# Kernel tuning notes

Measured on AMD Instinct MI355X. Metric: run time of the kernel, lower is better.

## Reference

```python
import jax, jax.numpy as jnp
import numpy as np

N, E = 50000, 800000
IN, HID, L, HEADS, OUT = 128, 256, 8, 8, 40
DH = HID // HEADS


def setup_inputs() -> dict:
    key = jax.random.key(0)
    ks = jax.random.split(key, 12)
    s = 0.05
    d = {}
    d["X"] = jax.random.normal(ks[0], (N, IN), jnp.float32)
    d["src"] = jax.random.randint(ks[1], (E,), 0, N, dtype=jnp.int32)
    d["dst"] = jax.random.randint(ks[2], (E,), 0, N, dtype=jnp.int32)
    d["Win"] = jax.random.normal(ks[3], (IN, HID), jnp.float32) * s
    d["bin_"] = jnp.zeros((HID,), jnp.float32)
    d["Wq"] = jax.random.normal(ks[4], (L, HID, HID), jnp.float32) * s
    d["Wk"] = jax.random.normal(ks[5], (L, HID, HID), jnp.float32) * s
    d["Wv"] = jax.random.normal(ks[6], (L, HID, HID), jnp.float32) * s
    d["bq"] = jnp.zeros((L, HID), jnp.float32)
    d["bk"] = jnp.zeros((L, HID), jnp.float32)
    d["bv"] = jnp.zeros((L, HID), jnp.float32)
    d["Wout"] = jax.random.normal(ks[7], (HID, OUT), jnp.float32) * s
    d["bout"] = jnp.zeros((OUT,), jnp.float32)
    return d


def _segment_softmax(e, seg, n):
    # e: [E, H] edge scores, seg: [E] destination node ids
    m = jax.ops.segment_max(e, seg, num_segments=n)
    ex = jnp.exp(e - m[seg])
    s = jax.ops.segment_sum(ex, seg, num_segments=n)
    return ex / s[seg]


def reference(X, src, dst, Win, bin_, Wq, Wk, Wv, bq, bk, bv, Wout, bout):
    n = X.shape[0]
    scaling = DH ** -0.5
    h = X @ Win + bin_  # in_proj: [N, HID]
    for l in range(L):  # fixed small layer stack
        q = (h @ Wq[l] + bq[l]).reshape(n, HEADS, DH) * scaling
        k = (h @ Wk[l] + bk[l]).reshape(n, HEADS, DH)
        v = (h @ Wv[l] + bv[l]).reshape(n, HEADS, DH)
        # SDDMM: per-edge, per-head dot product q[dst] . k[src]
        e = jnp.einsum('ehd,ehd->eh', q[dst], k[src])  # [E, HEADS]
        a = _segment_softmax(e, dst, n)                # softmax over in-edges of each dst
        # SpMM: weighted aggregation of source values into destinations
        h = jax.ops.segment_sum(a[..., None] * v[src], dst, num_segments=n).reshape(n, HID)
    return h @ Wout + bout  # predictor: [N, OUT]
```

## Files before the change

### kernel.cpp

```cpp
#include <hip/hip_runtime.h>
#include <hip/hip_bf16.h>
#include <hip/hip_fp16.h>

#define N_NODES 50000
#define MPAD    50048
#define N_EDGES 800000
#define IN_DIM  128
#define HID     256
#define QKVW    768
#define N_LAYERS 8
#define OUT_DIM 40
#define SCALING 0.17677669529663687f

typedef __attribute__((ext_vector_type(8))) _Float16 f16x8;
typedef __attribute__((ext_vector_type(4))) float f32x4;

__device__ __forceinline__ void gload_lds16(const void* g, void* l) {
    __builtin_amdgcn_global_load_lds(
        (__attribute__((address_space(1))) const unsigned int*)g,
        (__attribute__((address_space(3))) unsigned int*)l, 16, 0, 0);
}

__global__ void hist_kernel(const int* __restrict__ dst, int* __restrict__ cnt, int E) {
    int e = blockIdx.x * blockDim.x + threadIdx.x;
    if (e < E) atomicAdd(&cnt[dst[e]], 1);
}

__global__ __launch_bounds__(1024) void scan_kernel(const int* __restrict__ cnt,
                                                    int* __restrict__ row_off, int n) {
    __shared__ int wsum[16];
    __shared__ int carry_s;
    int tid = threadIdx.x;
    int lane = tid & 63, wid = tid >> 6;
    if (tid == 0) carry_s = 0;
    __syncthreads();
    for (int base = 0; base < n; base += 1024) {
        int i = base + tid;
        int x = (i < n) ? cnt[i] : 0;
        int v = x;
#pragma unroll
        for (int off = 1; off < 64; off <<= 1) {
            int y = __shfl_up(v, off);
            if (lane >= off) v += y;
        }
        if (lane == 63) wsum[wid] = v;
        __syncthreads();
        if (wid == 0) {
            int w = (lane < 16) ? wsum[lane] : 0;
#pragma unroll
            for (int off = 1; off < 16; off <<= 1) {
                int y = __shfl_up(w, off);
                if (lane >= off) w += y;
            }
            if (lane < 16) wsum[lane] = w;
        }
        __syncthreads();
        int wbase = (wid > 0) ? wsum[wid - 1] : 0;
        int carry = carry_s;
        if (i < n) row_off[i] = carry + wbase + v - x;
        int total = wsum[15];
        __syncthreads();
        if (tid == 0) carry_s = carry + total;
        __syncthreads();
    }
    if (tid == 0) row_off[n] = carry_s;
}

__global__ void scatter_kernel(const int* __restrict__ src, const int* __restrict__ dst,
                               const int* __restrict__ row_off, int* __restrict__ cur,
                               int* __restrict__ csr_src, int E) {
    int e = blockIdx.x * blockDim.x + threadIdx.x;
    if (e < E) {
        int d = dst[e];
        int pos = row_off[d] + atomicAdd(&cur[d], 1);
        csr_src[pos] = src[e];
    }
}

__global__ void wqkv_cvt_kernel(const float* __restrict__ Wq, const float* __restrict__ Wk,
                                const float* __restrict__ Wv, _Float16* __restrict__ outw) {
    int i = blockIdx.x * blockDim.x + threadIdx.x;
    if (i >= N_LAYERS * QKVW * HID) return;
    int k = i & 255;
    int n = (i >> 8) % QKVW;
    int l = i / (QKVW * HID);
    int seg = n >> 8, nn = n & 255;
    const float* W = (seg == 0) ? Wq : (seg == 1) ? Wk : Wv;
    outw[i] = (_Float16)W[((size_t)l * HID + k) * HID + nn];
}

__global__ void win_cvt_kernel(const float* __restrict__ Win, _Float16* __restrict__ outw) {
    int i = blockIdx.x * blockDim.x + threadIdx.x;
    if (i >= HID * IN_DIM) return;
    int k = i & 127;
    int n = i >> 7;
    outw[i] = (_Float16)Win[(size_t)k * HID + n];
}

__global__ void wout_cvt_kernel(const float* __restrict__ Wout, _Float16* __restrict__ hi,
                                _Float16* __restrict__ lo) {
    int i = blockIdx.x * blockDim.x + threadIdx.x;
    if (i >= 128 * HID) return;
    int k = i & 255;
    int n = i >> 8;
    float v = (n < OUT_DIM) ? Wout[(size_t)k * OUT_DIM + n] : 0.f;
    _Float16 h = (_Float16)v;
    hi[i] = h;
    lo[i] = (_Float16)(v - (float)h);
}

__global__ void x_cvt_kernel(const float* __restrict__ X, _Float16* __restrict__ outx) {
    int i = blockIdx.x * blockDim.x + threadIdx.x;
    if (i >= MPAD * IN_DIM) return;
    int r = i >> 7;
    outx[i] = (_Float16)((r < N_NODES) ? X[i] : 0.f);
}

template<int NT>
__global__ __launch_bounds__(256) void gemm16(
        const _Float16* __restrict__ A, const _Float16* __restrict__ B,
        const float* __restrict__ bias0, const float* __restrict__ bias1,
        const float* __restrict__ bias2, float scale0,
        _Float16* __restrict__ C, int ldC) {
    __shared__ __align__(16) _Float16 lds[2][2 * 4096];
    const int K = NT * 32;

    const int tid  = threadIdx.x;
    const int lane = tid & 63;
    const int wave = tid >> 6;
    const int row0 = blockIdx.x * 128;
    const int n0   = blockIdx.y * 128;

    const int p0 = wave * 64 + lane;
    const int p1 = p0 + 256;
    auto srcoff = [&](int p, int grow0) -> size_t {
        int row = p >> 2, cir = p & 3;
        int sw  = (row & 3) ^ ((row >> 2) & 3);
        int sc  = cir ^ sw;
        return (size_t)(grow0 + row) * K + sc * 8;
    };
    const size_t offA0 = srcoff(p0, row0), offA1 = srcoff(p1, row0);
    const size_t offB0 = srcoff(p0, n0),   offB1 = srcoff(p1, n0);
    const int d0 = wave * 512;
    const int d1 = 2048 + wave * 512;

    const int mh = (wave >> 1) * 64;
    const int nh = (wave & 1) * 64;
    int aoff[4], boff[4];
#pragma unroll
    for (int f = 0; f < 4; ++f) {
        int ra = mh + f * 16 + (lane & 15);
        int ca = (lane >> 4) ^ ((ra & 3) ^ ((ra >> 2) & 3));
        aoff[f] = ra * 64 + ca * 16;
        int rb = nh + f * 16 + (lane & 15);
        int cb = (lane >> 4) ^ ((rb & 3) ^ ((rb >> 2) & 3));
        boff[f] = rb * 64 + cb * 16;
    }

    f32x4 acc[4][4];
#pragma unroll
    for (int i = 0; i < 4; ++i)
#pragma unroll
        for (int j = 0; j < 4; ++j) acc[i][j] = {0.f, 0.f, 0.f, 0.f};

    auto STAGE = [&](int b, int t) {
        _Float16* LA = &lds[b][0];
        _Float16* LB = &lds[b][4096];
        const size_t k0 = (size_t)t * 32;
        gload_lds16(A + offA0 + k0, LA + d0);
        gload_lds16(A + offA1 + k0, LA + d1);
        gload_lds16(B + offB0 + k0, LB + d0);
        gload_lds16(B + offB1 + k0, LB + d1);
    };

    STAGE(0, 0);
#pragma unroll
    for (int t = 0; t < NT; ++t) {
        const int cur = t & 1;
        if (t + 1 < NT) {
            STAGE(cur ^ 1, t + 1);
            asm volatile("s_waitcnt vmcnt(4)" ::: "memory");
        } else {
            asm volatile("s_waitcnt vmcnt(0)" ::: "memory");
        }
        __builtin_amdgcn_s_barrier();
        const char* baseA = (const char*)&lds[cur][0];
        const char* baseB = (const char*)&lds[cur][4096];
        f16x8 af[4];
#pragma unroll
        for (int i = 0; i < 4; ++i)
            af[i] = *reinterpret_cast<const f16x8*>(baseA + aoff[i]);
#pragma unroll
        for (int j = 0; j < 4; ++j) {
            f16x8 bf = *reinterpret_cast<const f16x8*>(baseB + boff[j]);
#pragma unroll
            for (int i = 0; i < 4; ++i)
                acc[i][j] = __builtin_amdgcn_mfma_f32_16x16x32_f16(af[i], bf, acc[i][j], 0, 0, 0);
        }
        __builtin_amdgcn_s_barrier();
    }

    const int seg = n0 >> 8;
    const float* bias = (seg == 0) ? bias0 : (seg == 1) ? bias1 : bias2;
    const float scale = (seg == 0) ? scale0 : 1.f;
    const int fq = lane >> 4;
    const int fr = lane & 15;
#pragma unroll
    for (int i = 0; i < 4; ++i) {
#pragma unroll
        for (int j = 0; j < 4; ++j) {
#pragma unroll
            for (int r = 0; r < 4; ++r) {
                int m = row0 + mh + i * 16 + fq * 4 + r;
                int n = n0 + nh + j * 16 + fr;
                float o = (acc[i][j][r] + bias[n & 255]) * scale;
                C[(size_t)m * ldC + n] = (_Float16)o;
            }
        }
    }
}

__global__ __launch_bounds__(256) void gemm_out(
        const _Float16* __restrict__ A, const _Float16* __restrict__ Bh,
        const _Float16* __restrict__ Bl, const float* __restrict__ bias,
        float* __restrict__ C, int K) {
    __shared__ __align__(16) _Float16 lds[2][3 * 4096];

    const int tid  = threadIdx.x;
    const int lane = tid & 63;
    const int wave = tid >> 6;
    const int row0 = blockIdx.x * 128;

    const int p0 = wave * 64 + lane;
    const int p1 = p0 + 256;
    auto srcoff = [&](int p, int grow0) -> size_t {
        int row = p >> 2, cir = p & 3;
        int sw  = (row & 3) ^ ((row >> 2) & 3);
        int sc  = cir ^ sw;
        return (size_t)(grow0 + row) * K + sc * 8;
    };
    const size_t offA0 = srcoff(p0, row0), offA1 = srcoff(p1, row0);
    const size_t offB0 = srcoff(p0, 0),    offB1 = srcoff(p1, 0);
    const int d0 = wave * 512;
    const int d1 = 2048 + wave * 512;

    const int mh = (wave >> 1) * 64;
    const int nh = (wave & 1) * 64;
    int aoff[4], boff[4];
#pragma unroll
    for (int f = 0; f < 4; ++f) {
        int ra = mh + f * 16 + (lane & 15);
        int ca = (lane >> 4) ^ ((ra & 3) ^ ((ra >> 2) & 3));
        aoff[f] = ra * 64 + ca * 16;
        int rb = nh + f * 16 + (lane & 15);
        int cb = (lane >> 4) ^ ((rb & 3) ^ ((rb >> 2) & 3));
        boff[f] = rb * 64 + cb * 16;
    }

    f32x4 acc[4][4];
#pragma unroll
    for (int i = 0; i < 4; ++i)
#pragma unroll
        for (int j = 0; j < 4; ++j) acc[i][j] = {0.f, 0.f, 0.f, 0.f};

    auto STAGE = [&](int b, int t) {
        _Float16* LA  = &lds[b][0];
        _Float16* LBh = &lds[b][4096];
        _Float16* LBl = &lds[b][8192];
        const size_t k0 = (size_t)t * 32;
        gload_lds16(A  + offA0 + k0, LA  + d0);
        gload_lds16(A  + offA1 + k0, LA  + d1);
        gload_lds16(Bh + offB0 + k0, LBh + d0);
        gload_lds16(Bh + offB1 + k0, LBh + d1);
        gload_lds16(Bl + offB0 + k0, LBl + d0);
        gload_lds16(Bl + offB1 + k0, LBl + d1);
    };

    STAGE(0, 0);
#pragma unroll
    for (int t = 0; t < 8; ++t) {
        const int cur = t & 1;
        if (t + 1 < 8) {
            STAGE(cur ^ 1, t + 1);
            asm volatile("s_waitcnt vmcnt(6)" ::: "memory");
        } else {
            asm volatile("s_waitcnt vmcnt(0)" ::: "memory");
        }
        __builtin_amdgcn_s_barrier();
        const char* baseA  = (const char*)&lds[cur][0];
        const char* baseBh = (const char*)&lds[cur][4096];
        const char* baseBl = (const char*)&lds[cur][8192];
        f16x8 af[4];
#pragma unroll
        for (int i = 0; i < 4; ++i)
            af[i] = *reinterpret_cast<const f16x8*>(baseA + aoff[i]);
#pragma unroll
        for (int j = 0; j < 4; ++j) {
            f16x8 bh = *reinterpret_cast<const f16x8*>(baseBh + boff[j]);
            f16x8 bl = *reinterpret_cast<const f16x8*>(baseBl + boff[j]);
#pragma unroll
            for (int i = 0; i < 4; ++i) {
                acc[i][j] = __builtin_amdgcn_mfma_f32_16x16x32_f16(af[i], bh, acc[i][j], 0, 0, 0);
                acc[i][j] = __builtin_amdgcn_mfma_f32_16x16x32_f16(af[i], bl, acc[i][j], 0, 0, 0);
            }
        }
        __builtin_amdgcn_s_barrier();
    }

    const int fq = lane >> 4;
    const int fr = lane & 15;
#pragma unroll
    for (int i = 0; i < 4; ++i) {
#pragma unroll
        for (int j = 0; j < 4; ++j) {
#pragma unroll
            for (int r = 0; r < 4; ++r) {
                int m = row0 + mh + i * 16 + fq * 4 + r;
                int n = nh + j * 16 + fr;
                if (m < N_NODES && n < OUT_DIM)
                    C[(size_t)m * OUT_DIM + n] = acc[i][j][r] + bias[n];
            }
        }
    }
}

__global__ __launch_bounds__(256) void attn_kernel(
        const _Float16* __restrict__ qkv, const int* __restrict__ row_off,
        const int* __restrict__ csr_src, _Float16* __restrict__ h_out, int n) {
    int wave = threadIdx.x >> 6;
    int lane = threadIdx.x & 63;
    int node = blockIdx.x * 4 + wave;
    if (node >= n) return;
    const int loff = lane * 4;
    float4 qv;
    {
        float2 raw = *reinterpret_cast<const float2*>(&qkv[(size_t)node * QKVW + loff]);
        const __half2* h2 = reinterpret_cast<const __half2*>(&raw);
        float2 a = __half22float2(h2[0]), b = __half22float2(h2[1]);
        qv = make_float4(a.x, a.y, b.x, b.y);
    }
    float4 acc = make_float4(0.f, 0.f, 0.f, 0.f);
    float m = -INFINITY, s = 0.f;
    int beg = row_off[node], end = row_off[node + 1];
    int idx = beg;

#define LOAD_KV(slot, sn)                                                                 \
    float2 kr##slot, vr##slot;                                                            \
    {                                                                                     \
        const _Float16* base = qkv + (size_t)(sn) * QKVW;                                 \
        kr##slot = *reinterpret_cast<const float2*>(base + HID + loff);                   \
        vr##slot = *reinterpret_cast<const float2*>(base + 2 * HID + loff);               \
    }

#define DOT(slot, dvar)                                                                   \
    float dvar;                                                                           \
    {                                                                                     \
        const __half2* kh = reinterpret_cast<const __half2*>(&kr##slot);                  \
        float2 k01 = __half22float2(kh[0]), k23 = __half22float2(kh[1]);                  \
        dvar = qv.x * k01.x + qv.y * k01.y + qv.z * k23.x + qv.w * k23.y;                 \
        dvar += __shfl_xor(dvar, 1);                                                      \
        dvar += __shfl_xor(dvar, 2);                                                      \
        dvar += __shfl_xor(dvar, 4);                                                      \
    }

#define VADD(slot, p)                                                                     \
    {                                                                                     \
        const __half2* vh = reinterpret_cast<const __half2*>(&vr##slot);                  \
        float2 v01 = __half22float2(vh[0]), v23 = __half22float2(vh[1]);                  \
        acc.x = fmaf(p, v01.x, acc.x);                                                    \
        acc.y = fmaf(p, v01.y, acc.y);                                                    \
        acc.z = fmaf(p, v23.x, acc.z);                                                    \
        acc.w = fmaf(p, v23.y, acc.w);                                                    \
    }

    for (; idx + 3 < end; idx += 4) {
        int s0 = csr_src[idx], s1 = csr_src[idx + 1];
        int s2 = csr_src[idx + 2], s3 = csr_src[idx + 3];
        LOAD_KV(0, s0) LOAD_KV(1, s1) LOAD_KV(2, s2) LOAD_KV(3, s3)
        DOT(0, e0) DOT(1, e1) DOT(2, e2) DOT(3, e3)
        float mn = fmaxf(fmaxf(fmaxf(m, e0), fmaxf(e1, e2)), e3);
        float c  = __expf(m - mn);
        float p0 = __expf(e0 - mn), p1 = __expf(e1 - mn);
        float p2 = __expf(e2 - mn), p3 = __expf(e3 - mn);
        s = fmaf(s, c, (p0 + p1) + (p2 + p3));
        acc.x *= c; acc.y *= c; acc.z *= c; acc.w *= c;
        VADD(0, p0) VADD(1, p1) VADD(2, p2) VADD(3, p3)
        m = mn;
    }
    for (; idx < end; ++idx) {
        int s0 = csr_src[idx];
        LOAD_KV(0, s0)
        DOT(0, e0)
        float mn = fmaxf(m, e0);
        float c = __expf(m - mn);
        float p0 = __expf(e0 - mn);
        s = fmaf(s, c, p0);
        acc.x *= c; acc.y *= c; acc.z *= c; acc.w *= c;
        VADD(0, p0)
        m = mn;
    }
#undef LOAD_KV
#undef DOT
#undef VADD

    float inv = (s > 0.f) ? 1.f / s : 0.f;
    __half2 o01 = __floats2half2_rn(acc.x * inv, acc.y * inv);
    __half2 o23 = __floats2half2_rn(acc.z * inv, acc.w * inv);
    union { __half2 h2[2]; float2 f2; } u;
    u.h2[0] = o01; u.h2[1] = o23;
    *reinterpret_cast<float2*>(&h_out[(size_t)node * HID + loff]) = u.f2;
}

extern "C" void kernel_launch(void* const* d_in, const int* in_sizes, int n_in,
                              void* d_out, int out_size, void* d_ws, size_t ws_size,
                              hipStream_t stream) {
    const float* X    = (const float*)d_in[0];
    const int*   src  = (const int*)d_in[1];
    const int*   dst  = (const int*)d_in[2];
    const float* Win  = (const float*)d_in[3];
    const float* bin_ = (const float*)d_in[4];
    const float* Wq   = (const float*)d_in[5];
    const float* Wk   = (const float*)d_in[6];
    const float* Wv   = (const float*)d_in[7];
    const float* bq   = (const float*)d_in[8];
    const float* bk   = (const float*)d_in[9];
    const float* bv   = (const float*)d_in[10];
    const float* Wout = (const float*)d_in[11];
    const float* bout = (const float*)d_in[12];
    float* out = (float*)d_out;

    char* ws = (char*)d_ws;
    size_t off = 0;
    auto alloc = [&](size_t bytes) -> void* {
        void* p = ws + off;
        off = (off + bytes + 255) & ~(size_t)255;
        return p;
    };
    _Float16* qkv   = (_Float16*)alloc((size_t)MPAD * QKVW * 2);
    _Float16* h     = (_Float16*)alloc((size_t)MPAD * HID * 2);
    _Float16* Xf    = (_Float16*)alloc((size_t)MPAD * IN_DIM * 2);
    _Float16* Wqkvt = (_Float16*)alloc((size_t)N_LAYERS * QKVW * HID * 2);
    _Float16* Wint  = (_Float16*)alloc((size_t)HID * IN_DIM * 2);
    _Float16* Wot_h = (_Float16*)alloc((size_t)128 * HID * 2);
    _Float16* Wot_l = (_Float16*)alloc((size_t)128 * HID * 2);
    int* cnt     = (int*)alloc(sizeof(int) * N_NODES);
    int* row_off = (int*)alloc(sizeof(int) * (N_NODES + 1));
    int* csr_src = (int*)alloc(sizeof(int) * N_EDGES);

    hipMemsetAsync(cnt, 0, sizeof(int) * N_NODES, stream);
    hist_kernel<<<(N_EDGES + 255) / 256, 256, 0, stream>>>(dst, cnt, N_EDGES);
    scan_kernel<<<1, 1024, 0, stream>>>(cnt, row_off, N_NODES);
    hipMemsetAsync(cnt, 0, sizeof(int) * N_NODES, stream);
    scatter_kernel<<<(N_EDGES + 255) / 256, 256, 0, stream>>>(src, dst, row_off, cnt, csr_src, N_EDGES);

    {
        int t1 = N_LAYERS * QKVW * HID;
        wqkv_cvt_kernel<<<(t1 + 255) / 256, 256, 0, stream>>>(Wq, Wk, Wv, Wqkvt);
        int t2 = HID * IN_DIM;
        win_cvt_kernel<<<(t2 + 255) / 256, 256, 0, stream>>>(Win, Wint);
        int t3 = 128 * HID;
        wout_cvt_kernel<<<(t3 + 255) / 256, 256, 0, stream>>>(Wout, Wot_h, Wot_l);
        int t4 = MPAD * IN_DIM;
        x_cvt_kernel<<<(t4 + 255) / 256, 256, 0, stream>>>(X, Xf);
    }

    dim3 blk(256);
    gemm16<4><<<dim3(MPAD / 128, 2), blk, 0, stream>>>(
        Xf, Wint, bin_, bin_, bin_, 1.f, h, HID);

    for (int l = 0; l < N_LAYERS; ++l) {
        const _Float16* Bl = Wqkvt + (size_t)l * QKVW * HID;
        gemm16<8><<<dim3(MPAD / 128, 6), blk, 0, stream>>>(
            h, Bl, bq + l * HID, bk + l * HID, bv + l * HID, SCALING, qkv, QKVW);
        attn_kernel<<<(N_NODES + 3) / 4, blk, 0, stream>>>(
            qkv, row_off, csr_src, h, N_NODES);
    }
    gemm_out<<<dim3(MPAD / 128, 1), blk, 0, stream>>>(
        h, Wot_h, Wot_l, bout, out, HID);
}
```

Measured before the change: 1.518 ms.

## Interleave K/V columns, sort CSR neighbours by source, remap GEMM block order

The QKV GEMM now writes K and V interleaved per column, so the attention kernel fetches both for a neighbour with one 16-byte load instead of two 8-byte loads. A new resort kernel buckets each node's neighbour list by source-id range (warp ballot) for better gather locality. The GEMM grid is flattened with a swizzle that groups 8 row blocks per column tile, aiming for L2 reuse of B, and padded blocks are skipped. Together these add a preprocessing pass, extra workspace and more complex index math.

Result: no change. 1.526 ms (+0.5%).

```diff
diff --git a/kernel.cpp b/kernel.cpp
--- a/kernel.cpp
+++ b/kernel.cpp
@@ -4,6 +4,7 @@
 
 #define N_NODES 50000
 #define MPAD    50048
+#define NRB     391
 #define N_EDGES 800000
 #define IN_DIM  128
 #define HID     256
@@ -77,6 +78,31 @@
     }
 }
 
+__global__ __launch_bounds__(256) void resort_kernel(
+        const int* __restrict__ row_off, const int* __restrict__ csr_in,
+        int* __restrict__ csr_out, int n) {
+    int wave = threadIdx.x >> 6, lane = threadIdx.x & 63;
+    int node = blockIdx.x * 4 + wave;
+    if (node >= n) return;
+    int beg = row_off[node], end = row_off[node + 1];
+    int deg = end - beg;
+    if (deg <= 64) {
+        int sv = (lane < deg) ? csr_in[beg + lane] : 0;
+        int b  = (lane < deg) ? (sv >> 10) : 63;
+        int base = 0;
+        for (int t = 0; t < 49; ++t) {
+            unsigned long long mask = __ballot(b == t);
+            if (b == t) {
+                int pre = __popcll(mask & ((1ull << lane) - 1ull));
+                csr_out[beg + base + pre] = sv;
+            }
+            base += __popcll(mask);
+        }
+    } else {
+        for (int i = beg + lane; i < end; i += 64) csr_out[i] = csr_in[i];
+    }
+}
+
 __global__ void wqkv_cvt_kernel(const float* __restrict__ Wq, const float* __restrict__ Wk,
                                 const float* __restrict__ Wv, _Float16* __restrict__ outw) {
     int i = blockIdx.x * blockDim.x + threadIdx.x;
@@ -116,7 +142,7 @@
     outx[i] = (_Float16)((r < N_NODES) ? X[i] : 0.f);
 }
 
-template<int NT>
+template<int NT, int NCOLT, bool KVILV>
 __global__ __launch_bounds__(256) void gemm16(
         const _Float16* __restrict__ A, const _Float16* __restrict__ B,
         const float* __restrict__ bias0, const float* __restrict__ bias1,
@@ -125,11 +151,17 @@
     __shared__ __align__(16) _Float16 lds[2][2 * 4096];
     const int K = NT * 32;
 
+    const int bb = blockIdx.x;
+    const int xx = bb & 7, tt = bb >> 3;
+    const int qq = tt / NCOLT, jj = tt - qq * NCOLT;
+    const int rowblk = qq * 8 + xx;
+    if (rowblk >= NRB) return;
+    const int row0 = rowblk * 128;
+    const int n0   = jj * 128;
+
     const int tid  = threadIdx.x;
     const int lane = tid & 63;
     const int wave = tid >> 6;
-    const int row0 = blockIdx.x * 128;
-    const int n0   = blockIdx.y * 128;
 
     const int p0 = wave * 64 + lane;
     const int p1 = p0 + 256;
@@ -214,7 +246,9 @@
                 int m = row0 + mh + i * 16 + fq * 4 + r;
                 int n = n0 + nh + j * 16 + fr;
                 float o = (acc[i][j][r] + bias[n & 255]) * scale;
-                C[(size_t)m * ldC + n] = (_Float16)o;
+                int col = n;
+                if (KVILV && n >= 256) col = 256 + 2 * (n & 255) + (n >= 512 ? 1 : 0);
+                C[(size_t)m * ldC + col] = (_Float16)o;
             }
         }
     }
@@ -322,6 +356,28 @@
             }
         }
     }
+}
+
+struct KVf { float2 p0, p1, p2, p3; };
+__device__ __forceinline__ KVf unpack_kv(const float4& r) {
+    const __half2* h = reinterpret_cast<const __half2*>(&r);
+    KVf o;
+    o.p0 = __half22float2(h[0]); o.p1 = __half22float2(h[1]);
+    o.p2 = __half22float2(h[2]); o.p3 = __half22float2(h[3]);
+    return o;
+}
+__device__ __forceinline__ float dot_kv(const float4& q, const KVf& kv) {
+    float d = q.x * kv.p0.x + q.y * kv.p1.x + q.z * kv.p2.x + q.w * kv.p3.x;
+    d += __shfl_xor(d, 1);
+    d += __shfl_xor(d, 2);
+    d += __shfl_xor(d, 4);
+    return d;
+}
+__device__ __forceinline__ void vadd_kv(float4& acc, float p, const KVf& kv) {
+    acc.x = fmaf(p, kv.p0.y, acc.x);
+    acc.y = fmaf(p, kv.p1.y, acc.y);
+    acc.z = fmaf(p, kv.p2.y, acc.z);
+    acc.w = fmaf(p, kv.p3.y, acc.w);
 }
 
 __global__ __launch_bounds__(256) void attn_kernel(
@@ -343,65 +399,42 @@
     float m = -INFINITY, s = 0.f;
     int beg = row_off[node], end = row_off[node + 1];
     int idx = beg;
-
-#define LOAD_KV(slot, sn)                                                                 \
-    float2 kr##slot, vr##slot;                                                            \
-    {                                                                                     \
-        const _Float16* base = qkv + (size_t)(sn) * QKVW;                                 \
-        kr##slot = *reinterpret_cast<const float2*>(base + HID + loff);                   \
-        vr##slot = *reinterpret_cast<const float2*>(base + 2 * HID + loff);               \
-    }
-
-#define DOT(slot, dvar)                                                                   \
-    float dvar;                                                                           \
-    {                                                                                     \
-        const __half2* kh = reinterpret_cast<const __half2*>(&kr##slot);                  \
-        float2 k01 = __half22float2(kh[0]), k23 = __half22float2(kh[1]);                  \
-        dvar = qv.x * k01.x + qv.y * k01.y + qv.z * k23.x + qv.w * k23.y;                 \
-        dvar += __shfl_xor(dvar, 1);                                                      \
-        dvar += __shfl_xor(dvar, 2);                                                      \
-        dvar += __shfl_xor(dvar, 4);                                                      \
-    }
-
-#define VADD(slot, p)                                                                     \
-    {                                                                                     \
-        const __half2* vh = reinterpret_cast<const __half2*>(&vr##slot);                  \
-        float2 v01 = __half22float2(vh[0]), v23 = __half22float2(vh[1]);                  \
-        acc.x = fmaf(p, v01.x, acc.x);                                                    \
-        acc.y = fmaf(p, v01.y, acc.y);                                                    \
-        acc.z = fmaf(p, v23.x, acc.z);                                                    \
-        acc.w = fmaf(p, v23.y, acc.w);                                                    \
-    }
+    const int koff = HID + 2 * loff;
 
     for (; idx + 3 < end; idx += 4) {
         int s0 = csr_src[idx], s1 = csr_src[idx + 1];
         int s2 = csr_src[idx + 2], s3 = csr_src[idx + 3];
-        LOAD_KV(0, s0) LOAD_KV(1, s1) LOAD_KV(2, s2) LOAD_KV(3, s3)
-        DOT(0, e0) DOT(1, e1) DOT(2, e2) DOT(3, e3)
+        float4 r0 = *(const float4*)(qkv + (size_t)s0 * QKVW + koff);
+        float4 r1 = *(const float4*)(qkv + (size_t)s1 * QKVW + koff);
+        float4 r2 = *(const float4*)(qkv + (size_t)s2 * QKVW + koff);
+        float4 r3 = *(const float4*)(qkv + (size_t)s3 * QKVW + koff);
+        KVf kv0 = unpack_kv(r0), kv1 = unpack_kv(r1);
+        KVf kv2 = unpack_kv(r2), kv3 = unpack_kv(r3);
+        float e0 = dot_kv(qv, kv0), e1 = dot_kv(qv, kv1);
+        float e2 = dot_kv(qv, kv2), e3 = dot_kv(qv, kv3);
         float mn = fmaxf(fmaxf(fmaxf(m, e0), fmaxf(e1, e2)), e3);
         float c  = __expf(m - mn);
         float p0 = __expf(e0 - mn), p1 = __expf(e1 - mn);
         float p2 = __expf(e2 - mn), p3 = __expf(e3 - mn);
         s = fmaf(s, c, (p0 + p1) + (p2 + p3));
         acc.x *= c; acc.y *= c; acc.z *= c; acc.w *= c;
-        VADD(0, p0) VADD(1, p1) VADD(2, p2) VADD(3, p3)
+        vadd_kv(acc, p0, kv0); vadd_kv(acc, p1, kv1);
+        vadd_kv(acc, p2, kv2); vadd_kv(acc, p3, kv3);
         m = mn;
     }
     for (; idx < end; ++idx) {
         int s0 = csr_src[idx];
-        LOAD_KV(0, s0)
-        DOT(0, e0)
+        float4 r0 = *(const float4*)(qkv + (size_t)s0 * QKVW + koff);
+        KVf kv0 = unpack_kv(r0);
+        float e0 = dot_kv(qv, kv0);
         float mn = fmaxf(m, e0);
         float c = __expf(m - mn);
         float p0 = __expf(e0 - mn);
         s = fmaf(s, c, p0);
         acc.x *= c; acc.y *= c; acc.z *= c; acc.w *= c;
-        VADD(0, p0)
+        vadd_kv(acc, p0, kv0);
         m = mn;
     }
-#undef LOAD_KV
-#undef DOT
-#undef VADD
 
     float inv = (s > 0.f) ? 1.f / s : 0.f;
     __half2 o01 = __floats2half2_rn(acc.x * inv, acc.y * inv);
@@ -445,13 +478,15 @@
     _Float16* Wot_l = (_Float16*)alloc((size_t)128 * HID * 2);
     int* cnt     = (int*)alloc(sizeof(int) * N_NODES);
     int* row_off = (int*)alloc(sizeof(int) * (N_NODES + 1));
-    int* csr_src = (int*)alloc(sizeof(int) * N_EDGES);
+    int* csr_tmp = (int*)alloc(sizeof(int) * N_EDGES);
+    int* csr_srt = (int*)alloc(sizeof(int) * N_EDGES);
 
     hipMemsetAsync(cnt, 0, sizeof(int) * N_NODES, stream);
     hist_kernel<<<(N_EDGES + 255) / 256, 256, 0, stream>>>(dst, cnt, N_EDGES);
     scan_kernel<<<1, 1024, 0, stream>>>(cnt, row_off, N_NODES);
     hipMemsetAsync(cnt, 0, sizeof(int) * N_NODES, stream);
-    scatter_kernel<<<(N_EDGES + 255) / 256, 256, 0, stream>>>(src, dst, row_off, cnt, csr_src, N_EDGES);
+    scatter_kernel<<<(N_EDGES + 255) / 256, 256, 0, stream>>>(src, dst, row_off, cnt, csr_tmp, N_EDGES);
+    resort_kernel<<<(N_NODES + 3) / 4, 256, 0, stream>>>(row_off, csr_tmp, csr_srt, N_NODES);
 
     {
         int t1 = N_LAYERS * QKVW * HID;
@@ -465,16 +500,17 @@
     }
 
     dim3 blk(256);
-    gemm16<4><<<dim3(MPAD / 128, 2), blk, 0, stream>>>(
+    const int NQ = 8 * ((NRB + 7) / 8);
+    gemm16<4, 2, false><<<dim3(NQ * 2), blk, 0, stream>>>(
         Xf, Wint, bin_, bin_, bin_, 1.f, h, HID);
 
     for (int l = 0; l < N_LAYERS; ++l) {
         const _Float16* Bl = Wqkvt + (size_t)l * QKVW * HID;
-        gemm16<8><<<dim3(MPAD / 128, 6), blk, 0, stream>>>(
+        gemm16<8, 6, true><<<dim3(NQ * 6), blk, 0, stream>>>(
             h, Bl, bq + l * HID, bk + l * HID, bv + l * HID, SCALING, qkv, QKVW);
         attn_kernel<<<(N_NODES + 3) / 4, blk, 0, stream>>>(
-            qkv, row_off, csr_src, h, N_NODES);
-    }
-    gemm_out<<<dim3(MPAD / 128, 1), blk, 0, stream>>>(
+            qkv, row_off, csr_srt, h, N_NODES);
+    }
+    gemm_out<<<dim3(NRB), blk, 0, stream>>>(
         h, Wot_h, Wot_l, bout, out, HID);
 }
```
